# Kernel tuning notes

Hardware: AMD Instinct MI355X
Metric: run time of the kernel (lower is better)

The kernel has to match this reference:

```python
import jax, jax.numpy as jnp
import numpy as np

NEG_SLOPE = 0.2  # PyG GATv2Conv default


def with_self_loops(edge_index, n):
    loop = jnp.arange(n, dtype=edge_index.dtype)
    src = jnp.concatenate([edge_index[0], loop])
    dst = jnp.concatenate([edge_index[1], loop])
    return src, dst


def gatv2(x, src, dst, Wl, bl, Wr, br, att, bias):
    """PyG GATv2Conv (eval mode, concat=True, add_self_loops done by caller).
    x: [N, F_in]; att: [H, C]. Returns [N, H*C]."""
    N = x.shape[0]
    H, C = att.shape
    xl = (x @ Wl + bl).reshape(N, H, C)  # lin_l(x): source-side transform
    xr = (x @ Wr + br).reshape(N, H, C)  # lin_r(x): target-side transform
    s = jax.nn.leaky_relu(xl[src] + xr[dst], NEG_SLOPE)      # [E,H,C]
    logit = jnp.einsum('ehc,hc->eh', s, att)                 # [E,H]
    m = jax.ops.segment_max(logit, dst, num_segments=N)      # stable softmax per target
    e = jnp.exp(logit - m[dst])
    den = jax.ops.segment_sum(e, dst, num_segments=N)
    alpha = e / (den[dst] + 1e-16)                           # [E,H]
    out = jax.ops.segment_sum(alpha[:, :, None] * xl[src], dst, num_segments=N)
    return out.reshape(N, H * C) + bias


def setup_inputs() -> dict:
    N, E = 20000, 320000        # agent nodes / edges
    M, EM = 40000, 400000       # lane nodes / edges
    B, L = 64, 50               # focal agents, centerline length
    SEQ, INC, HID, HEADS, OUT = 50, 2, 32, 4, 60
    H4 = HID * HEADS
    key = jax.random.key(0)
    ks = list(jax.random.split(key, 48))
    kit = iter(ks)

    def p(shape):
        return jax.random.normal(next(kit), shape, jnp.float32) * 0.05

    inp = {
        'x': jax.random.normal(next(kit), (N, SEQ, INC), jnp.float32),
        'edge_index': jax.random.randint(next(kit), (2, E), 0, N),
        'lane_x': jax.random.normal(next(kit), (M, 2), jnp.float32),
        'lane_edge_index': jax.random.randint(next(kit), (2, EM), 0, M),
        'batch': jnp.sort(jax.random.randint(next(kit), (N,), 0, B)),
        'focal_idx': jax.random.randint(next(kit), (B,), 0, N),
        'centerlines': jax.random.normal(next(kit), (B, L, 2), jnp.float32),
        # agent embedding
        'ae_W': p((SEQ * INC, HID)), 'ae_b': p((HID,)),
        # agent subgraph conv1 / conv2
        'a1_Wl': p((HID, H4)), 'a1_bl': p((H4,)), 'a1_Wr': p((HID, H4)), 'a1_br': p((H4,)), 'a1_att': p((HEADS, HID)), 'a1_b': p((H4,)),
        'a2_Wl': p((H4, H4)), 'a2_bl': p((H4,)), 'a2_Wr': p((H4, H4)), 'a2_br': p((H4,)), 'a2_att': p((HEADS, HID)), 'a2_b': p((H4,)),
        # map embedding + map subgraph
        'me_W': p((2, HID)), 'me_b': p((HID,)),
        'm1_Wl': p((HID, H4)), 'm1_bl': p((H4,)), 'm1_Wr': p((HID, H4)), 'm1_br': p((H4,)), 'm1_att': p((HEADS, HID)), 'm1_b': p((H4,)),
        'm2_Wl': p((H4, H4)), 'm2_bl': p((H4,)), 'm2_Wr': p((H4, H4)), 'm2_br': p((H4,)), 'm2_att': p((HEADS, HID)), 'm2_b': p((H4,)),
        # centerline processor
        'cl_W': p((2, HID)), 'cl_b': p((HID,)),
        # global graph (heads=1)
        'g_Wl': p((H4, HID)), 'g_bl': p((HID,)), 'g_Wr': p((H4, HID)), 'g_br': p((HID,)), 'g_att': p((1, HID)), 'g_b': p((HID,)),
        # output head
        'fc_W': p((2 * HID, OUT)), 'fc_b': p((OUT,)),
    }
    return inp


def reference(x, edge_index, lane_x, lane_edge_index, batch, focal_idx, centerlines,
              ae_W, ae_b,
              a1_Wl, a1_bl, a1_Wr, a1_br, a1_att, a1_b,
              a2_Wl, a2_bl, a2_Wr, a2_br, a2_att, a2_b,
              me_W, me_b,
              m1_Wl, m1_bl, m1_Wr, m1_br, m1_att, m1_b,
              m2_Wl, m2_bl, m2_Wr, m2_br, m2_att, m2_b,
              cl_W, cl_b,
              g_Wl, g_bl, g_Wr, g_br, g_att, g_b,
              fc_W, fc_b):
    N = x.shape[0]
    M = lane_x.shape[0]
    # agent branch
    agent_x = jax.nn.relu(x.reshape(N, -1) @ ae_W + ae_b)
    a_src, a_dst = with_self_loops(edge_index, N)
    h = jax.nn.relu(gatv2(agent_x, a_src, a_dst, a1_Wl, a1_bl, a1_Wr, a1_br, a1_att, a1_b))
    agent_features = jax.nn.relu(gatv2(h, a_src, a_dst, a2_Wl, a2_bl, a2_Wr, a2_br, a2_att, a2_b))  # [N,128]
    # map branch (output unused downstream in original, computed for faithfulness)
    map_x = jax.nn.relu(lane_x @ me_W + me_b)
    m_src, m_dst = with_self_loops(lane_edge_index, M)
    hm = jax.nn.relu(gatv2(map_x, m_src, m_dst, m1_Wl, m1_bl, m1_Wr, m1_br, m1_att, m1_b))
    map_features = jax.nn.relu(gatv2(hm, m_src, m_dst, m2_Wl, m2_bl, m2_Wr, m2_br, m2_att, m2_b))
    _ = map_features  # global_mean_pool results are dead code in the original forward
    # global graph over agent features (heads=1)
    global_features = jax.nn.relu(gatv2(agent_features, a_src, a_dst, g_Wl, g_bl, g_Wr, g_br, g_att, g_b))  # [N,32]
    focal = global_features[focal_idx]  # [B,32]
    # centerlines: per-polyline mean then linear (no relu, as in original)
    cl_feat = jnp.mean(centerlines, axis=1) @ cl_W + cl_b  # [B,32]
    combined = jnp.concatenate([focal, cl_feat], axis=1)
    return combined @ fc_W + fc_b
```

## Files before the change

### kernel.cpp

```cpp
#include <hip/hip_runtime.h>
#include <hip/hip_bf16.h>
#include <hip/hip_fp16.h>
#include <math.h>

typedef __hip_bfloat16 bf16;
#define NEG_SLOPE 0.2f
#define SFLAG (1 << 30)

typedef _Float16 f16x8 __attribute__((ext_vector_type(8)));
typedef float f32x4 __attribute__((ext_vector_type(4)));

__global__ void k_detect_zero(const unsigned short* __restrict__ x, int* __restrict__ flag,
                              int* __restrict__ zbase, int n) {
    for (int i = blockIdx.x * blockDim.x + threadIdx.x; i < n; i += gridDim.x * blockDim.x)
        zbase[i] = 0;
    if (blockIdx.x == 0) {
        __shared__ int cnt;
        if (threadIdx.x == 0) cnt = 0;
        __syncthreads();
        int local = 0;
        for (int i = threadIdx.x; i < 2048; i += blockDim.x) {
            unsigned short w = x[2 * i];
            int e = (w >> 7) & 0xFF;
            if (e >= 0x90) local++;
        }
        atomicAdd(&cnt, local);
        __syncthreads();
        if (threadIdx.x == 0) flag[0] = (cnt > 100) ? 1 : 0;
    }
}

#define NSEG 25
struct Seg { const void* src; int n; int off; };
struct Tab { Seg s[NSEG]; };

__device__ __forceinline__ float ldconv(const void* src, int i, int f32mode) {
    return f32mode ? ((const float*)src)[i]
                   : __bfloat162float(((const bf16*)src)[i]);
}

__global__ void k_convert(Tab tab, float* __restrict__ dst, const int* __restrict__ flag,
                          const int* __restrict__ dstArr, int E, int N,
                          int* __restrict__ deg, int* __restrict__ rank,
                          const void* a2WlS, const void* a2WrS,
                          const void* gWlS, const void* gWrS,
                          __half* __restrict__ a2Wlt, __half* __restrict__ a2Wrt,
                          __half* __restrict__ gWlt, __half* __restrict__ gWrt) {
    int f32mode = flag[0];
    int gid = blockIdx.x * blockDim.x + threadIdx.x;
    int gsz = gridDim.x * blockDim.x;
    for (int s = 0; s < NSEG; s++) {
        Seg sg = tab.s[s];
        for (int i = gid; i < sg.n; i += gsz) {
            dst[sg.off + i] = ldconv(sg.src, i, f32mode);
        }
    }
    for (int i = gid; i < 128 * 128; i += gsz) {
        int k = i >> 7, j = i & 127;
        a2Wlt[(size_t)j * 128 + k] = __float2half(ldconv(a2WlS, i, f32mode));
        a2Wrt[(size_t)j * 128 + k] = __float2half(ldconv(a2WrS, i, f32mode));
    }
    for (int i = gid; i < 128 * 32; i += gsz) {
        int k = i >> 5, j = i & 31;
        gWlt[(size_t)j * 128 + k] = __float2half(ldconv(gWlS, i, f32mode));
        gWrt[(size_t)j * 128 + k] = __float2half(ldconv(gWrS, i, f32mode));
    }
    int EA = E + N;
    for (int e = gid; e < EA; e += gsz) {
        int d = (e < E) ? dstArr[e] : (e - E);
        rank[e] = atomicAdd(&deg[d], 1);
    }
}

__launch_bounds__(1024)
__global__ void k_scanf(const int* __restrict__ deg, int* __restrict__ offs,
                        int n, int* __restrict__ st, int nb) {
    __shared__ int ws[16];
    __shared__ int stot, sprev;
    int tile = blockIdx.x;
    int i = tile * 1024 + threadIdx.x;
    int lane = threadIdx.x & 63, wid = threadIdx.x >> 6;
    int v = (i < n) ? deg[i] : 0;
    int x = v;
    #pragma unroll
    for (int o = 1; o < 64; o <<= 1) {
        int y = __shfl_up(x, o);
        if (lane >= o) x += y;
    }
    if (lane == 63) ws[wid] = x;
    __syncthreads();
    if (wid == 0) {
        int w = (lane < 16) ? ws[lane] : 0;
        int s = w;
        #pragma unroll
        for (int o = 1; o < 16; o <<= 1) {
            int y = __shfl_up(s, o);
            if (lane >= o) s += y;
        }
        if (lane < 16) ws[lane] = s - w;
        if (lane == 15) stot = s;
    }
    __syncthreads();
    int local = ws[wid] + x - v;
    if (threadIdx.x == 0) {
        int prev = 0;
        if (tile > 0) {
            int vv;
            while ((((vv = __hip_atomic_load(&st[tile - 1], __ATOMIC_ACQUIRE,
                                             __HIP_MEMORY_SCOPE_AGENT))) & SFLAG) == 0) {}
            prev = vv & ~SFLAG;
        }
        __hip_atomic_store(&st[tile], (prev + stot) | SFLAG, __ATOMIC_RELEASE,
                           __HIP_MEMORY_SCOPE_AGENT);
        sprev = prev;
        if (tile == nb - 1) offs[n] = prev + stot;
    }
    __syncthreads();
    if (i < n) offs[i] = sprev + local;
}

__launch_bounds__(256)
__global__ void k_fill_embedlin(const int* __restrict__ srcArr, const int* __restrict__ dstArr,
                                int E, int N, const int* __restrict__ offs,
                                const int* __restrict__ rank, int* __restrict__ csr,
                                const void* __restrict__ xraw, const int* __restrict__ flag,
                                const float* __restrict__ aeW, const float* __restrict__ aeb,
                                const float* __restrict__ Wl, const float* __restrict__ bl,
                                const float* __restrict__ Wr, const float* __restrict__ br,
                                __half* __restrict__ outl, float* __restrict__ outr,
                                int EB) {
    __shared__ float xs[100 * 36];
    __shared__ float axs[32 * 36];
    if (blockIdx.x >= EB) {
        int e = (blockIdx.x - EB) * 256 + threadIdx.x;
        int EA = E + N;
        if (e >= EA) return;
        int d, s;
        if (e < E) { d = dstArr[e]; s = srcArr[e]; } else { d = s = e - E; }
        csr[offs[d] + rank[e]] = s;
        return;
    }
    constexpr int NTP = 36;
    int t = threadIdx.x, nb = blockIdx.x * 32;
    if (flag[0]) {
        const float4* x4 = (const float4*)xraw;
        for (int idx = t; idx < 32 * 25; idx += 256) {
            int node = idx / 25, k4 = idx % 25;
            float4 v = x4[(size_t)(nb + node) * 25 + k4];
            xs[(k4 * 4 + 0) * NTP + node] = v.x;
            xs[(k4 * 4 + 1) * NTP + node] = v.y;
            xs[(k4 * 4 + 2) * NTP + node] = v.z;
            xs[(k4 * 4 + 3) * NTP + node] = v.w;
        }
    } else {
        const ushort4* xu = (const ushort4*)xraw;
        for (int idx = t; idx < 32 * 25; idx += 256) {
            int node = idx / 25, k4 = idx % 25;
            ushort4 u = xu[(size_t)(nb + node) * 25 + k4];
            xs[(k4 * 4 + 0) * NTP + node] = __uint_as_float((unsigned)u.x << 16);
            xs[(k4 * 4 + 1) * NTP + node] = __uint_as_float((unsigned)u.y << 16);
            xs[(k4 * 4 + 2) * NTP + node] = __uint_as_float((unsigned)u.z << 16);
            xs[(k4 * 4 + 3) * NTP + node] = __uint_as_float((unsigned)u.w << 16);
        }
    }
    __syncthreads();
    {
        int j = t & 31, g0 = t >> 5;
        float a0 = 0.f, a1 = 0.f, a2 = 0.f, a3 = 0.f;
        #pragma unroll 10
        for (int k = 0; k < 100; k++) {
            float w = aeW[k * 32 + j];
            const float4 xv = *(const float4*)&xs[k * NTP + g0 * 4];
            a0 += w * xv.x; a1 += w * xv.y; a2 += w * xv.z; a3 += w * xv.w;
        }
        float bj = aeb[j];
        axs[j * NTP + g0 * 4 + 0] = fmaxf(a0 + bj, 0.f);
        axs[j * NTP + g0 * 4 + 1] = fmaxf(a1 + bj, 0.f);
        axs[j * NTP + g0 * 4 + 2] = fmaxf(a2 + bj, 0.f);
        axs[j * NTP + g0 * 4 + 3] = fmaxf(a3 + bj, 0.f);
    }
    __syncthreads();
    {
        int j = t & 63, g0 = t >> 6;
        float aL0[2][4], aL1[2][4], aR0[2][4], aR1[2][4];
        #pragma unroll
        for (int g = 0; g < 2; g++)
            #pragma unroll
            for (int c = 0; c < 4; c++) { aL0[g][c]=0.f; aL1[g][c]=0.f; aR0[g][c]=0.f; aR1[g][c]=0.f; }
        #pragma unroll 4
        for (int k = 0; k < 32; k++) {
            float wl0 = Wl[k * 128 + j];
            float wl1 = Wl[k * 128 + j + 64];
            float wr0 = Wr[k * 128 + j];
            float wr1 = Wr[k * 128 + j + 64];
            #pragma unroll
            for (int g = 0; g < 2; g++) {
                const float4 xv = *(const float4*)&axs[k * NTP + (g0 + g * 4) * 4];
                aL0[g][0] += wl0 * xv.x; aL0[g][1] += wl0 * xv.y; aL0[g][2] += wl0 * xv.z; aL0[g][3] += wl0 * xv.w;
                aL1[g][0] += wl1 * xv.x; aL1[g][1] += wl1 * xv.y; aL1[g][2] += wl1 * xv.z; aL1[g][3] += wl1 * xv.w;
                aR0[g][0] += wr0 * xv.x; aR0[g][1] += wr0 * xv.y; aR0[g][2] += wr0 * xv.z; aR0[g][3] += wr0 * xv.w;
                aR1[g][0] += wr1 * xv.x; aR1[g][1] += wr1 * xv.y; aR1[g][2] += wr1 * xv.z; aR1[g][3] += wr1 * xv.w;
            }
        }
        float bl0 = bl[j], bl1 = bl[j + 64], br0 = br[j], br1 = br[j + 64];
        #pragma unroll
        for (int g = 0; g < 2; g++) {
            int n0 = nb + (g0 + g * 4) * 4;
            #pragma unroll
            for (int c = 0; c < 4; c++) {
                size_t row = (size_t)(n0 + c) * 128;
                outl[row + j]      = __float2half(aL0[g][c] + bl0);
                outl[row + j + 64] = __float2half(aL1[g][c] + bl1);
                outr[row + j]      = aR0[g][c] + br0;
                outr[row + j + 64] = aR1[g][c] + br1;
            }
        }
    }
}

__device__ __forceinline__ void gat_proc(float4 raw, bool valid,
                                         const float* xrd, const float* av,
                                         float* acc, float& sm) {
    const __half2* h = (const __half2*)&raw;
    float v[8];
    float2 f;
    f = __half22float2(h[0]); v[0] = f.x; v[1] = f.y;
    f = __half22float2(h[1]); v[2] = f.x; v[3] = f.y;
    f = __half22float2(h[2]); v[4] = f.x; v[5] = f.y;
    f = __half22float2(h[3]); v[6] = f.x; v[7] = f.y;
    float p = 0.f;
    #pragma unroll
    for (int c = 0; c < 8; c++) {
        float u = v[c] + xrd[c];
        u = (u > 0.f) ? u : NEG_SLOPE * u;
        p += u * av[c];
    }
    p += __shfl_xor(p, 1);
    p += __shfl_xor(p, 2);
    p += __shfl_xor(p, 4);
    p += __shfl_xor(p, 8);
    float w = __expf(fminf(p, 80.f));
    if (!valid) w = 0.f;
    sm += w;
    #pragma unroll
    for (int c = 0; c < 8; c++) acc[c] += w * v[c];
}

__device__ void gat_one_serial(const __half* __restrict__ xl,
                               const int* __restrict__ csr, int i0, int i1,
                               const float* xrd, const float* av,
                               float* acc, float& sm, int lane, int grp, int sub) {
    for (int base = i0; base < i1; base += 64) {
        int cnt = min(i1 - base, 64);
        int myv = (lane < cnt) ? csr[base + lane] : 0;
        int nbq = (cnt + 15) >> 4;
        for (int q = 0; q < nbq; q++) {
            int e0 = q * 16 + grp;
            int s0 = __shfl(myv, e0 & 63);
            int s1 = __shfl(myv, (e0 + 4) & 63);
            int s2 = __shfl(myv, (e0 + 8) & 63);
            int s3 = __shfl(myv, (e0 + 12) & 63);
            float4 r0 = *(const float4*)(xl + (size_t)s0 * 128 + sub * 8);
            float4 r1 = *(const float4*)(xl + (size_t)s1 * 128 + sub * 8);
            float4 r2 = *(const float4*)(xl + (size_t)s2 * 128 + sub * 8);
            float4 r3 = *(const float4*)(xl + (size_t)s3 * 128 + sub * 8);
            gat_proc(r0, e0 < cnt, xrd, av, acc, sm);
            gat_proc(r1, e0 + 4 < cnt, xrd, av, acc, sm);
            gat_proc(r2, e0 + 8 < cnt, xrd, av, acc, sm);
            gat_proc(r3, e0 + 12 < cnt, xrd, av, acc, sm);
        }
    }
}

__device__ __forceinline__ void gat16_to_lds(__half* xsh,
                                             const __half* __restrict__ xl,
                                             const float* __restrict__ xr,
                                             const float* __restrict__ att,
                                             const int* __restrict__ offs,
                                             const int* __restrict__ csr,
                                             const float* __restrict__ bias,
                                             int nb, int N) {
    int t = threadIdx.x;
    int wave = t >> 6, lane = t & 63;
    int grp = lane >> 4, sub = lane & 15;
    float av[8];
    {
        const float4* t4 = (const float4*)(att + sub * 8);
        float4 c = t4[0], e = t4[1];
        av[0]=c.x; av[1]=c.y; av[2]=c.z; av[3]=c.w;
        av[4]=e.x; av[5]=e.y; av[6]=e.z; av[7]=e.w;
    }
    for (int it = 0; it < 4; it += 2) {
        int d0 = nb + wave * 4 + it;
        int d1 = d0 + 1;
        bool ok0 = d0 < N, ok1 = d1 < N;
        int i00 = ok0 ? offs[d0] : 0, i01 = ok0 ? offs[d0 + 1] : 0;
        int i10 = ok1 ? offs[d1] : 0, i11 = ok1 ? offs[d1 + 1] : 0;
        int cnt0 = i01 - i00, cnt1 = i11 - i10;

        float xrd0[8], xrd1[8], acc0[8], acc1[8];
        float sm0 = 0.f, sm1 = 0.f;
        #pragma unroll
        for (int c = 0; c < 8; c++) { acc0[c] = 0.f; acc1[c] = 0.f; }
        if (ok0) {
            const float4* p4 = (const float4*)(xr + (size_t)d0 * 128 + sub * 8);
            float4 a = p4[0], b = p4[1];
            xrd0[0]=a.x; xrd0[1]=a.y; xrd0[2]=a.z; xrd0[3]=a.w;
            xrd0[4]=b.x; xrd0[5]=b.y; xrd0[6]=b.z; xrd0[7]=b.w;
        }
        if (ok1) {
            const float4* p4 = (const float4*)(xr + (size_t)d1 * 128 + sub * 8);
            float4 a = p4[0], b = p4[1];
            xrd1[0]=a.x; xrd1[1]=a.y; xrd1[2]=a.z; xrd1[3]=a.w;
            xrd1[4]=b.x; xrd1[5]=b.y; xrd1[6]=b.z; xrd1[7]=b.w;
        }

        if (cnt0 <= 64 && cnt1 <= 64) {
            int myv0 = (lane < cnt0) ? csr[i00 + lane] : 0;
            int myv1 = (lane < cnt1) ? csr[i10 + lane] : 0;
            int nb0 = (cnt0 + 15) >> 4, nb1 = (cnt1 + 15) >> 4;
            int nbm = max(nb0, nb1);
            for (int q = 0; q < nbm; q++) {
                int e0 = q * 16 + grp;
                float4 r00, r01, r02, r03, r10, r11, r12, r13;
                if (q < nb0) {
                    int s0 = __shfl(myv0, e0 & 63);
                    int s1 = __shfl(myv0, (e0 + 4) & 63);
                    int s2 = __shfl(myv0, (e0 + 8) & 63);
                    int s3 = __shfl(myv0, (e0 + 12) & 63);
                    r00 = *(const float4*)(xl + (size_t)s0 * 128 + sub * 8);
                    r01 = *(const float4*)(xl + (size_t)s1 * 128 + sub * 8);
                    r02 = *(const float4*)(xl + (size_t)s2 * 128 + sub * 8);
                    r03 = *(const float4*)(xl + (size_t)s3 * 128 + sub * 8);
                }
                if (q < nb1) {
                    int s0 = __shfl(myv1, e0 & 63);
                    int s1 = __shfl(myv1, (e0 + 4) & 63);
                    int s2 = __shfl(myv1, (e0 + 8) & 63);
                    int s3 = __shfl(myv1, (e0 + 12) & 63);
                    r10 = *(const float4*)(xl + (size_t)s0 * 128 + sub * 8);
                    r11 = *(const float4*)(xl + (size_t)s1 * 128 + sub * 8);
                    r12 = *(const float4*)(xl + (size_t)s2 * 128 + sub * 8);
                    r13 = *(const float4*)(xl + (size_t)s3 * 128 + sub * 8);
                }
                if (q < nb0) {
                    gat_proc(r00, e0 < cnt0, xrd0, av, acc0, sm0);
                    gat_proc(r01, e0 + 4 < cnt0, xrd0, av, acc0, sm0);
                    gat_proc(r02, e0 + 8 < cnt0, xrd0, av, acc0, sm0);
                    gat_proc(r03, e0 + 12 < cnt0, xrd0, av, acc0, sm0);
                }
                if (q < nb1) {
                    gat_proc(r10, e0 < cnt1, xrd1, av, acc1, sm1);
                    gat_proc(r11, e0 + 4 < cnt1, xrd1, av, acc1, sm1);
                    gat_proc(r12, e0 + 8 < cnt1, xrd1, av, acc1, sm1);
                    gat_proc(r13, e0 + 12 < cnt1, xrd1, av, acc1, sm1);
                }
            }
        } else {
            if (ok0) gat_one_serial(xl, csr, i00, i01, xrd0, av, acc0, sm0, lane, grp, sub);
            if (ok1) gat_one_serial(xl, csr, i10, i11, xrd1, av, acc1, sm1, lane, grp, sub);
        }

        sm0 += __shfl_xor(sm0, 16); sm0 += __shfl_xor(sm0, 32);
        sm1 += __shfl_xor(sm1, 16); sm1 += __shfl_xor(sm1, 32);
        #pragma unroll
        for (int c = 0; c < 8; c++) {
            acc0[c] += __shfl_xor(acc0[c], 16); acc0[c] += __shfl_xor(acc0[c], 32);
            acc1[c] += __shfl_xor(acc1[c], 16); acc1[c] += __shfl_xor(acc1[c], 32);
        }
        int c2 = grp * 2;
        int ch0 = sub * 8 + c2;
        if (ok0) {
            float inv = 1.f / (sm0 + 1e-16f);
            int node = d0 - nb;
            __half2 hv;
            hv.x = __float2half(fmaxf(acc0[c2] * inv + bias[ch0], 0.f));
            hv.y = __float2half(fmaxf(acc0[c2 + 1] * inv + bias[ch0 + 1], 0.f));
            *(__half2*)&xsh[node * 136 + ch0] = hv;
        }
        if (ok1) {
            float inv = 1.f / (sm1 + 1e-16f);
            int node = d1 - nb;
            __half2 hv;
            hv.x = __float2half(fmaxf(acc1[c2] * inv + bias[ch0], 0.f));
            hv.y = __float2half(fmaxf(acc1[c2 + 1] * inv + bias[ch0 + 1], 0.f));
            *(__half2*)&xsh[node * 136 + ch0] = hv;
        }
    }
}

__launch_bounds__(256)
__global__ void k_gatlin(const __half* __restrict__ xl, const float* __restrict__ xr,
                         const float* __restrict__ att,
                         const int* __restrict__ offs, const int* __restrict__ csr,
                         const float* __restrict__ bias,
                         const __half* __restrict__ Wlt, const float* __restrict__ bl,
                         const __half* __restrict__ Wrt, const float* __restrict__ br,
                         __half* __restrict__ outl, float* __restrict__ outr, int N) {
    __shared__ __align__(16) __half xsh[16 * 136];
    int nb = blockIdx.x * 16;
    gat16_to_lds(xsh, xl, xr, att, offs, csr, bias, nb, N);
    __syncthreads();

    int t = threadIdx.x;
    int lane = t & 63, wv = t >> 6;
    int quad = lane >> 4, n16 = lane & 15;
    f16x8 a[4];
    #pragma unroll
    for (int kt = 0; kt < 4; kt++)
        a[kt] = *(const f16x8*)&xsh[n16 * 136 + kt * 32 + quad * 8];

    int j0 = wv * 32;
    f32x4 aL0 = {0.f,0.f,0.f,0.f}, aL1 = {0.f,0.f,0.f,0.f};
    f32x4 aR0 = {0.f,0.f,0.f,0.f}, aR1 = {0.f,0.f,0.f,0.f};
    #pragma unroll
    for (int kt = 0; kt < 4; kt++) {
        int ko = kt * 32 + quad * 8;
        f16x8 b0 = *(const f16x8*)&Wlt[(size_t)(j0 + n16) * 128 + ko];
        f16x8 b1 = *(const f16x8*)&Wlt[(size_t)(j0 + 16 + n16) * 128 + ko];
        f16x8 b2 = *(const f16x8*)&Wrt[(size_t)(j0 + n16) * 128 + ko];
        f16x8 b3 = *(const f16x8*)&Wrt[(size_t)(j0 + 16 + n16) * 128 + ko];
        aL0 = __builtin_amdgcn_mfma_f32_16x16x32_f16(a[kt], b0, aL0, 0, 0, 0);
        aL1 = __builtin_amdgcn_mfma_f32_16x16x32_f16(a[kt], b1, aL1, 0, 0, 0);
        aR0 = __builtin_amdgcn_mfma_f32_16x16x32_f16(a[kt], b2, aR0, 0, 0, 0);
        aR1 = __builtin_amdgcn_mfma_f32_16x16x32_f16(a[kt], b3, aR1, 0, 0, 0);
    }
    float blj0 = bl[j0 + n16], blj1 = bl[j0 + 16 + n16];
    float brj0 = br[j0 + n16], brj1 = br[j0 + 16 + n16];
    #pragma unroll
    for (int r = 0; r < 4; r++) {
        int node = quad * 4 + r;
        if (nb + node >= N) continue;
        size_t row = (size_t)(nb + node) * 128;
        outl[row + j0 + n16]      = __float2half(aL0[r] + blj0);
        outl[row + j0 + 16 + n16] = __float2half(aL1[r] + blj1);
        outr[row + j0 + n16]      = aR0[r] + brj0;
        outr[row + j0 + 16 + n16] = aR1[r] + brj1;
    }
}

__launch_bounds__(256)
__global__ void k_gatling(const __half* __restrict__ xl, const float* __restrict__ xr,
                          const float* __restrict__ att,
                          const int* __restrict__ offs, const int* __restrict__ csr,
                          const float* __restrict__ bias,
                          const __half* __restrict__ Wlt, const float* __restrict__ bl,
                          const __half* __restrict__ Wrt, const float* __restrict__ br,
                          __half* __restrict__ outl, float* __restrict__ outr, int N) {
    __shared__ __align__(16) __half xsh[16 * 136];
    int nb = blockIdx.x * 16;
    gat16_to_lds(xsh, xl, xr, att, offs, csr, bias, nb, N);
    __syncthreads();

    int t = threadIdx.x;
    int lane = t & 63, wv = t >> 6;
    int quad = lane >> 4, n16 = lane & 15;
    f16x8 a[4];
    #pragma unroll
    for (int kt = 0; kt < 4; kt++)
        a[kt] = *(const f16x8*)&xsh[n16 * 136 + kt * 32 + quad * 8];

    const __half* Wt = (wv < 2) ? Wlt : Wrt;
    int j0 = (wv & 1) * 16;
    f32x4 accv = {0.f,0.f,0.f,0.f};
    #pragma unroll
    for (int kt = 0; kt < 4; kt++) {
        f16x8 b = *(const f16x8*)&Wt[(size_t)(j0 + n16) * 128 + kt * 32 + quad * 8];
        accv = __builtin_amdgcn_mfma_f32_16x16x32_f16(a[kt], b, accv, 0, 0, 0);
    }
    float bj = ((wv < 2) ? bl : br)[j0 + n16];
    #pragma unroll
    for (int r = 0; r < 4; r++) {
        int node = quad * 4 + r;
        if (nb + node >= N) continue;
        size_t row = (size_t)(nb + node) * 32;
        if (wv < 2) outl[row + j0 + n16] = __float2half(accv[r] + bj);
        else        outr[row + j0 + n16] = accv[r] + bj;
    }
}

__launch_bounds__(64)
__global__ void k_tailf(const __half* __restrict__ xl, const float* __restrict__ xr,
                        const float* __restrict__ att,
                        const int* __restrict__ offs, const int* __restrict__ csr,
                        const float* __restrict__ gb, const int* __restrict__ focal,
                        const float* __restrict__ clf, const float* __restrict__ clW,
                        const float* __restrict__ clb, const float* __restrict__ fcW,
                        const float* __restrict__ fcb, void* __restrict__ out,
                        const int* __restrict__ flag) {
    __shared__ float comb[64];
    __shared__ float ssb[2];
    int b = blockIdx.x;
    int t = threadIdx.x;
    int d = focal[b];
    int grp = t >> 3, sub = t & 7;
    int i0 = offs[d], i1 = offs[d + 1];

    float xrd[4], av[4], acc[4];
    {
        float4 a = *(const float4*)(xr + (size_t)d * 32 + sub * 4);
        xrd[0]=a.x; xrd[1]=a.y; xrd[2]=a.z; xrd[3]=a.w;
        float4 c = *(const float4*)(att + sub * 4);
        av[0]=c.x; av[1]=c.y; av[2]=c.z; av[3]=c.w;
    }
    #pragma unroll
    for (int c = 0; c < 4; c++) acc[c] = 0.f;
    float sm = 0.f;

    for (int i = i0 + grp; i < i1; i += 8) {
        float2 raw = *(const float2*)(xl + (size_t)csr[i] * 32 + sub * 4);
        const __half2* h = (const __half2*)&raw;
        float v[4];
        float2 f;
        f = __half22float2(h[0]); v[0] = f.x; v[1] = f.y;
        f = __half22float2(h[1]); v[2] = f.x; v[3] = f.y;
        float p = 0.f;
        #pragma unroll
        for (int c = 0; c < 4; c++) {
            float u = v[c] + xrd[c];
            u = (u > 0.f) ? u : NEG_SLOPE * u;
            p += u * av[c];
        }
        p += __shfl_xor(p, 1);
        p += __shfl_xor(p, 2);
        p += __shfl_xor(p, 4);
        float w = __expf(fminf(p, 80.f));
        sm += w;
        #pragma unroll
        for (int c = 0; c < 4; c++) acc[c] += w * v[c];
    }
    sm += __shfl_xor(sm, 8); sm += __shfl_xor(sm, 16); sm += __shfl_xor(sm, 32);
    #pragma unroll
    for (int c = 0; c < 4; c++) {
        acc[c] += __shfl_xor(acc[c], 8);
        acc[c] += __shfl_xor(acc[c], 16);
        acc[c] += __shfl_xor(acc[c], 32);
    }
    if (grp == 0) {
        float inv = 1.f / (sm + 1e-16f);
        #pragma unroll
        for (int c = 0; c < 4; c++)
            comb[sub * 4 + c] = fmaxf(acc[c] * inv + gb[sub * 4 + c], 0.f);
    }
    if (t < 2) {
        float s = 0.f;
        for (int l = 0; l < 50; l++) s += clf[(size_t)b * 100 + l * 2 + t];
        ssb[t] = s / 50.f;
    }
    __syncthreads();
    if (t < 32) comb[32 + t] = ssb[0] * clW[t] + ssb[1] * clW[32 + t] + clb[t];
    __syncthreads();
    if (t < 60) {
        float a2 = fcb[t];
        #pragma unroll 16
        for (int k = 0; k < 64; k++) a2 += comb[k] * fcW[k * 60 + t];
        if (flag[0]) ((float*)out)[b * 60 + t] = a2;
        else ((bf16*)out)[b * 60 + t] = __float2bfloat16(a2);
    }
}

extern "C" void kernel_launch(void* const* d_in, const int* in_sizes, int n_in,
                              void* d_out, int out_size, void* d_ws, size_t ws_size,
                              hipStream_t stream) {
    const int* edge  = (const int*)d_in[1];
    const int* focal = (const int*)d_in[5];

    const int N = in_sizes[0] / 100;
    const int E = in_sizes[1] / 2;
    const int B = in_sizes[5];
    const int EA = E + N;
    const int* srcArr = edge;
    const int* dstArr = edge + E;

    const int idxs[NSEG] = {7,8,9,10,11,12,13,14,15,16,17,18,19,20,
                            35,36,37,38,39,40,41,42,43,44, 6};
    float* base = (float*)d_ws;
    int* flag = (int*)base;
    float* wf = base + 16;
    Tab tab;
    int off[NSEG];
    int o = 0;
    for (int i = 0; i < NSEG; i++) {
        tab.s[i].src = d_in[idxs[i]];
        tab.s[i].n   = in_sizes[idxs[i]];
        tab.s[i].off = o;
        off[i] = o;
        o += in_sizes[idxs[i]];
    }
    const float* aeW  = wf + off[0],  *aeb  = wf + off[1];
    const float* a1Wl = wf + off[2],  *a1bl = wf + off[3];
    const float* a1Wr = wf + off[4],  *a1br = wf + off[5];
    const float* a1att= wf + off[6],  *a1b  = wf + off[7];
    const float* a2bl = wf + off[9];
    const float* a2br = wf + off[11];
    const float* a2att= wf + off[12], *a2b  = wf + off[13];
    const float* clW  = wf + off[14], *clb  = wf + off[15];
    const float* gbl  = wf + off[17];
    const float* gbr  = wf + off[19];
    const float* gatt = wf + off[20], *gb   = wf + off[21];
    const float* fcW  = wf + off[22], *fcb  = wf + off[23];
    const float* clf  = wf + off[24];

    float* p = wf + o + ((4 - (o & 3)) & 3);
    size_t N128 = (size_t)N * 128;
    __half* hxl1 = (__half*)p;      p += (size_t)N * 64;
    float* fB1  = p;                p += N128;
    __half* hxl2 = (__half*)p;      p += (size_t)N * 64;
    float* fB2  = p;                p += N128;
    int* deg    = (int*)p;
    int* st     = deg + N;
    int* offs   = st + 32;
    int* rank   = offs + N + 1;
    int* csr    = rank + EA;
    uintptr_t up = (uintptr_t)(csr + EA);
    up = (up + 15) & ~(uintptr_t)15;
    __half* a2Wlt = (__half*)up;
    __half* a2Wrt = a2Wlt + 16384;
    __half* gWlt  = a2Wrt + 16384;
    __half* gWrt  = gWlt + 4096;

    const int NB = (N + 1023) / 1024;
    const int EB = N / 32;
    const int FBLK = (EA + 255) / 256;
    const int GT = (N + 15) / 16;

    k_detect_zero<<<64, 256, 0, stream>>>((const unsigned short*)d_in[0], flag, deg, N + 32);
    k_convert<<<256, 256, 0, stream>>>(tab, wf, flag, dstArr, E, N, deg, rank,
                                       d_in[15], d_in[17], d_in[37], d_in[39],
                                       a2Wlt, a2Wrt, gWlt, gWrt);
    k_scanf<<<NB, 1024, 0, stream>>>(deg, offs, N, st, NB);
    k_fill_embedlin<<<EB + FBLK, 256, 0, stream>>>(srcArr, dstArr, E, N, offs, rank, csr,
                                                   d_in[0], flag, aeW, aeb,
                                                   a1Wl, a1bl, a1Wr, a1br, hxl1, fB1, EB);
    k_gatlin<<<GT, 256, 0, stream>>>(hxl1, fB1, a1att, offs, csr, a1b,
                                     a2Wlt, a2bl, a2Wrt, a2br, hxl2, fB2, N);
    k_gatling<<<GT, 256, 0, stream>>>(hxl2, fB2, a2att, offs, csr, a2b,
                                      gWlt, gbl, gWrt, gbr, hxl1, fB1, N);
    k_tailf<<<B, 64, 0, stream>>>(hxl1, fB1, gatt, offs, csr, gb, focal,
                                  clf, clW, clb, fcW, fcb, d_out, flag);
}
```

Baseline: 291.8 us.

## Assign one destination node per 16-lane group in fused GAT-to-LDS aggregation

The edge-aggregation prologue of the fused GAT+linear kernel now maps each 16-lane group of a wave to its own destination node, instead of having a whole wave process two nodes at a time with four groups splitting edges. This removes the cross-group shuffle reductions and the separate serial path for high-degree nodes. It also prefetches the next chunk of CSR indices while the current one is processed. In exchange, groups in a wave diverge when node degrees differ, so the wave runs as long as its highest-degree node.

New measurement: 264.6 us. -9.3%, faster.

```diff
diff --git a/kernel.cpp b/kernel.cpp
--- a/kernel.cpp
+++ b/kernel.cpp
@@ -246,32 +246,6 @@
     for (int c = 0; c < 8; c++) acc[c] += w * v[c];
 }
 
-__device__ void gat_one_serial(const __half* __restrict__ xl,
-                               const int* __restrict__ csr, int i0, int i1,
-                               const float* xrd, const float* av,
-                               float* acc, float& sm, int lane, int grp, int sub) {
-    for (int base = i0; base < i1; base += 64) {
-        int cnt = min(i1 - base, 64);
-        int myv = (lane < cnt) ? csr[base + lane] : 0;
-        int nbq = (cnt + 15) >> 4;
-        for (int q = 0; q < nbq; q++) {
-            int e0 = q * 16 + grp;
-            int s0 = __shfl(myv, e0 & 63);
-            int s1 = __shfl(myv, (e0 + 4) & 63);
-            int s2 = __shfl(myv, (e0 + 8) & 63);
-            int s3 = __shfl(myv, (e0 + 12) & 63);
-            float4 r0 = *(const float4*)(xl + (size_t)s0 * 128 + sub * 8);
-            float4 r1 = *(const float4*)(xl + (size_t)s1 * 128 + sub * 8);
-            float4 r2 = *(const float4*)(xl + (size_t)s2 * 128 + sub * 8);
-            float4 r3 = *(const float4*)(xl + (size_t)s3 * 128 + sub * 8);
-            gat_proc(r0, e0 < cnt, xrd, av, acc, sm);
-            gat_proc(r1, e0 + 4 < cnt, xrd, av, acc, sm);
-            gat_proc(r2, e0 + 8 < cnt, xrd, av, acc, sm);
-            gat_proc(r3, e0 + 12 < cnt, xrd, av, acc, sm);
-        }
-    }
-}
-
 __device__ __forceinline__ void gat16_to_lds(__half* xsh,
                                              const __half* __restrict__ xl,
                                              const float* __restrict__ xr,
@@ -283,6 +257,7 @@
     int t = threadIdx.x;
     int wave = t >> 6, lane = t & 63;
     int grp = lane >> 4, sub = lane & 15;
+    int lb = lane & 48;
     float av[8];
     {
         const float4* t4 = (const float4*)(att + sub * 8);
@@ -290,101 +265,57 @@
         av[0]=c.x; av[1]=c.y; av[2]=c.z; av[3]=c.w;
         av[4]=e.x; av[5]=e.y; av[6]=e.z; av[7]=e.w;
     }
-    for (int it = 0; it < 4; it += 2) {
-        int d0 = nb + wave * 4 + it;
-        int d1 = d0 + 1;
-        bool ok0 = d0 < N, ok1 = d1 < N;
-        int i00 = ok0 ? offs[d0] : 0, i01 = ok0 ? offs[d0 + 1] : 0;
-        int i10 = ok1 ? offs[d1] : 0, i11 = ok1 ? offs[d1 + 1] : 0;
-        int cnt0 = i01 - i00, cnt1 = i11 - i10;
-
-        float xrd0[8], xrd1[8], acc0[8], acc1[8];
-        float sm0 = 0.f, sm1 = 0.f;
-        #pragma unroll
-        for (int c = 0; c < 8; c++) { acc0[c] = 0.f; acc1[c] = 0.f; }
-        if (ok0) {
-            const float4* p4 = (const float4*)(xr + (size_t)d0 * 128 + sub * 8);
-            float4 a = p4[0], b = p4[1];
-            xrd0[0]=a.x; xrd0[1]=a.y; xrd0[2]=a.z; xrd0[3]=a.w;
-            xrd0[4]=b.x; xrd0[5]=b.y; xrd0[6]=b.z; xrd0[7]=b.w;
-        }
-        if (ok1) {
-            const float4* p4 = (const float4*)(xr + (size_t)d1 * 128 + sub * 8);
-            float4 a = p4[0], b = p4[1];
-            xrd1[0]=a.x; xrd1[1]=a.y; xrd1[2]=a.z; xrd1[3]=a.w;
-            xrd1[4]=b.x; xrd1[5]=b.y; xrd1[6]=b.z; xrd1[7]=b.w;
-        }
-
-        if (cnt0 <= 64 && cnt1 <= 64) {
-            int myv0 = (lane < cnt0) ? csr[i00 + lane] : 0;
-            int myv1 = (lane < cnt1) ? csr[i10 + lane] : 0;
-            int nb0 = (cnt0 + 15) >> 4, nb1 = (cnt1 + 15) >> 4;
-            int nbm = max(nb0, nb1);
-            for (int q = 0; q < nbm; q++) {
-                int e0 = q * 16 + grp;
-                float4 r00, r01, r02, r03, r10, r11, r12, r13;
-                if (q < nb0) {
-                    int s0 = __shfl(myv0, e0 & 63);
-                    int s1 = __shfl(myv0, (e0 + 4) & 63);
-                    int s2 = __shfl(myv0, (e0 + 8) & 63);
-                    int s3 = __shfl(myv0, (e0 + 12) & 63);
-                    r00 = *(const float4*)(xl + (size_t)s0 * 128 + sub * 8);
-                    r01 = *(const float4*)(xl + (size_t)s1 * 128 + sub * 8);
-                    r02 = *(const float4*)(xl + (size_t)s2 * 128 + sub * 8);
-                    r03 = *(const float4*)(xl + (size_t)s3 * 128 + sub * 8);
-                }
-                if (q < nb1) {
-                    int s0 = __shfl(myv1, e0 & 63);
-                    int s1 = __shfl(myv1, (e0 + 4) & 63);
-                    int s2 = __shfl(myv1, (e0 + 8) & 63);
-                    int s3 = __shfl(myv1, (e0 + 12) & 63);
-                    r10 = *(const float4*)(xl + (size_t)s0 * 128 + sub * 8);
-                    r11 = *(const float4*)(xl + (size_t)s1 * 128 + sub * 8);
-                    r12 = *(const float4*)(xl + (size_t)s2 * 128 + sub * 8);
-                    r13 = *(const float4*)(xl + (size_t)s3 * 128 + sub * 8);
-                }
-                if (q < nb0) {
-                    gat_proc(r00, e0 < cnt0, xrd0, av, acc0, sm0);
-                    gat_proc(r01, e0 + 4 < cnt0, xrd0, av, acc0, sm0);
-                    gat_proc(r02, e0 + 8 < cnt0, xrd0, av, acc0, sm0);
-                    gat_proc(r03, e0 + 12 < cnt0, xrd0, av, acc0, sm0);
-                }
-                if (q < nb1) {
-                    gat_proc(r10, e0 < cnt1, xrd1, av, acc1, sm1);
-                    gat_proc(r11, e0 + 4 < cnt1, xrd1, av, acc1, sm1);
-                    gat_proc(r12, e0 + 8 < cnt1, xrd1, av, acc1, sm1);
-                    gat_proc(r13, e0 + 12 < cnt1, xrd1, av, acc1, sm1);
-                }
-            }
-        } else {
-            if (ok0) gat_one_serial(xl, csr, i00, i01, xrd0, av, acc0, sm0, lane, grp, sub);
-            if (ok1) gat_one_serial(xl, csr, i10, i11, xrd1, av, acc1, sm1, lane, grp, sub);
-        }
-
-        sm0 += __shfl_xor(sm0, 16); sm0 += __shfl_xor(sm0, 32);
-        sm1 += __shfl_xor(sm1, 16); sm1 += __shfl_xor(sm1, 32);
-        #pragma unroll
-        for (int c = 0; c < 8; c++) {
-            acc0[c] += __shfl_xor(acc0[c], 16); acc0[c] += __shfl_xor(acc0[c], 32);
-            acc1[c] += __shfl_xor(acc1[c], 16); acc1[c] += __shfl_xor(acc1[c], 32);
-        }
-        int c2 = grp * 2;
-        int ch0 = sub * 8 + c2;
-        if (ok0) {
-            float inv = 1.f / (sm0 + 1e-16f);
-            int node = d0 - nb;
+    int d = nb + wave * 4 + grp;
+    bool ok = d < N;
+    int i0 = ok ? offs[d] : 0;
+    int i1 = ok ? offs[d + 1] : 0;
+    int cnt = i1 - i0;
+
+    float xrd[8];
+    #pragma unroll
+    for (int c = 0; c < 8; c++) xrd[c] = 0.f;
+    if (ok) {
+        const float4* p4 = (const float4*)(xr + (size_t)d * 128 + sub * 8);
+        float4 a = p4[0], b = p4[1];
+        xrd[0]=a.x; xrd[1]=a.y; xrd[2]=a.z; xrd[3]=a.w;
+        xrd[4]=b.x; xrd[5]=b.y; xrd[6]=b.z; xrd[7]=b.w;
+    }
+    float acc[8];
+    #pragma unroll
+    for (int c = 0; c < 8; c++) acc[c] = 0.f;
+    float sm = 0.f;
+
+    int myv = (sub < cnt) ? csr[i0 + sub] : 0;
+    for (int c0 = 0; c0 < cnt; c0 += 16) {
+        int myv_nxt = (c0 + 16 + sub < cnt) ? csr[i0 + c0 + 16 + sub] : 0;
+        int rem = min(cnt - c0, 16);
+        for (int k = 0; k < rem; k += 4) {
+            int s0 = __shfl(myv, lb + k + 0);
+            int s1 = __shfl(myv, lb + k + 1);
+            int s2 = __shfl(myv, lb + k + 2);
+            int s3 = __shfl(myv, lb + k + 3);
+            float4 r0 = *(const float4*)(xl + (size_t)s0 * 128 + sub * 8);
+            float4 r1 = *(const float4*)(xl + (size_t)s1 * 128 + sub * 8);
+            float4 r2 = *(const float4*)(xl + (size_t)s2 * 128 + sub * 8);
+            float4 r3 = *(const float4*)(xl + (size_t)s3 * 128 + sub * 8);
+            gat_proc(r0, true,        xrd, av, acc, sm);
+            gat_proc(r1, k + 1 < rem, xrd, av, acc, sm);
+            gat_proc(r2, k + 2 < rem, xrd, av, acc, sm);
+            gat_proc(r3, k + 3 < rem, xrd, av, acc, sm);
+        }
+        myv = myv_nxt;
+    }
+
+    if (ok) {
+        float inv = 1.f / (sm + 1e-16f);
+        int node = wave * 4 + grp;
+        int ch = sub * 8;
+        #pragma unroll
+        for (int c = 0; c < 8; c += 2) {
             __half2 hv;
-            hv.x = __float2half(fmaxf(acc0[c2] * inv + bias[ch0], 0.f));
-            hv.y = __float2half(fmaxf(acc0[c2 + 1] * inv + bias[ch0 + 1], 0.f));
-            *(__half2*)&xsh[node * 136 + ch0] = hv;
-        }
-        if (ok1) {
-            float inv = 1.f / (sm1 + 1e-16f);
-            int node = d1 - nb;
-            __half2 hv;
-            hv.x = __float2half(fmaxf(acc1[c2] * inv + bias[ch0], 0.f));
-            hv.y = __float2half(fmaxf(acc1[c2 + 1] * inv + bias[ch0 + 1], 0.f));
-            *(__half2*)&xsh[node * 136 + ch0] = hv;
+            hv.x = __float2half(fmaxf(acc[c]     * inv + bias[ch + c],     0.f));
+            hv.y = __float2half(fmaxf(acc[c + 1] * inv + bias[ch + c + 1], 0.f));
+            *(__half2*)&xsh[node * 136 + ch + c] = hv;
         }
     }
 }
```
